# Optimization experiments

Measured on AMD Instinct MI355X. Metric: run time of the kernel, lower is better.

Reference implementation:

```python
import jax, jax.numpy as jnp
import numpy as np

CONV1_CH, CONV1_K = 8, 3
CONV2_CH, CONV2_K = 16, 2
DYN_POOL, MAX_POOL = 8, 4
FC1_IN, FC1_OUT = CONV2_CH * MAX_POOL * MAX_POOL, 100  # 256 -> 100


def k_max_pool(x, axis, k):
    # topk along axis, sort indices ascending, gather -> keeps original order of top-k
    xm = jnp.moveaxis(x, axis, -1)
    _, idx = jax.lax.top_k(xm, k)
    idx = jnp.sort(idx, axis=-1)
    out = jnp.take_along_axis(xm, idx, axis=-1)
    return jnp.moveaxis(out, -1, axis)


def _conv2d(x, w, b):
    y = jax.lax.conv_general_dilated(x, w, (1, 1), 'VALID',
                                     dimension_numbers=('NCHW', 'OIHW', 'NCHW'))
    return y + b[None, :, None, None]


def setup_inputs() -> dict:
    key = jax.random.key(0)
    ks = jax.random.split(key, 11)
    Lq, Ld, d, N = 128, 512, 64, 127
    inp = {
        'query': jax.random.normal(ks[0], (Lq, d), jnp.float32),
        'pos_doc': jax.random.normal(ks[1], (Ld, d), jnp.float32),
        'neg_docs': jax.random.normal(ks[2], (N, Ld, d), jnp.float32),
        'conv1_w': jax.random.normal(ks[3], (CONV1_CH, 1, CONV1_K, CONV1_K), jnp.float32) * 0.1,
        'conv1_b': jax.random.normal(ks[4], (CONV1_CH,), jnp.float32) * 0.1,
        'conv2_w': jax.random.normal(ks[5], (CONV2_CH, CONV1_CH, CONV2_K, CONV2_K), jnp.float32) * 0.1,
        'conv2_b': jax.random.normal(ks[6], (CONV2_CH,), jnp.float32) * 0.1,
        'lin1_w': jax.random.normal(ks[7], (FC1_OUT, FC1_IN), jnp.float32) * 0.05,
        'lin1_b': jax.random.normal(ks[8], (FC1_OUT,), jnp.float32) * 0.05,
        'lin2_w': jax.random.normal(ks[9], (1, FC1_OUT), jnp.float32) * 0.05,
        'lin2_b': jax.random.normal(ks[10], (1,), jnp.float32) * 0.05,
    }
    return inp


def reference(query, pos_doc, neg_docs, conv1_w, conv1_b, conv2_w, conv2_b,
              lin1_w, lin1_b, lin2_w, lin2_b):
    # Stack pos doc first, then negs (matches output stacking order in original)
    docs = jnp.concatenate([pos_doc[None], neg_docs], axis=0)      # [B, Ld, d]
    m = jnp.einsum('qd,bld->bql', query, docs)[:, None]            # [B, 1, Lq, Ld]
    # Layer 1: conv + relu + 2D k-max pooling to 8x8
    h = jax.nn.relu(_conv2d(m, conv1_w, conv1_b))                  # [B, 8, Lq-2, Ld-2]
    h = k_max_pool(h, 2, DYN_POOL)
    h = k_max_pool(h, 3, DYN_POOL)                                 # [B, 8, 8, 8]
    # Layer 2: conv + relu + 2D k-max pooling to 4x4
    h = jax.nn.relu(_conv2d(h, conv2_w, conv2_b))                  # [B, 16, 7, 7]
    h = k_max_pool(h, 2, MAX_POOL)
    h = k_max_pool(h, 3, MAX_POOL)                                 # [B, 16, 4, 4]
    feat = h.reshape(h.shape[0], -1)                               # [B, 256]
    z = jax.nn.relu(feat @ lin1_w.T + lin1_b)                      # [B, 100]
    s = jax.nn.relu(z @ lin2_w.T + lin2_b)                         # [B, 1]
    return s
```

## Files before the change

### kernel.cpp

```cpp
#include <hip/hip_runtime.h>
#include <cstdint>
#include <cstddef>

constexpr int kLq = 128;
constexpr int kLd = 512;
constexpr int kD  = 64;
constexpr int kB  = 128;
constexpr int kC1 = 8;
constexpr int kC2 = 16;
constexpr int kH1C = 510;
constexpr int kTileC = 51;
constexpr int kNTiles = 10;
constexpr int kMCols = 53;
constexpr int kNCand = kNTiles * 8;

constexpr int QT_PITCH = 132;
constexpr int DS_PITCH = 68;
constexpr int MS_PITCH = 57;

template <int K, bool LEX>
__device__ __forceinline__ void topk_insert(float (&tv)[K], int (&ti)[K],
                                            float v, int idx) {
  bool gK = LEX ? ((v > tv[K - 1]) | ((v == tv[K - 1]) & (idx < ti[K - 1])))
                : (v > tv[K - 1]);
  if (!gK) return;
  bool g[K];
#pragma unroll
  for (int k = 0; k < K; ++k)
    g[k] = LEX ? ((v > tv[k]) | ((v == tv[k]) & (idx < ti[k]))) : (v > tv[k]);
#pragma unroll
  for (int k = K - 1; k >= 1; --k) {
    tv[k] = g[k - 1] ? tv[k - 1] : (g[k] ? v : tv[k]);
    ti[k] = g[k - 1] ? ti[k - 1] : (g[k] ? idx : ti[k]);
  }
  if (g[0]) { tv[0] = v; ti[0] = idx; }
}

__global__ __launch_bounds__(512, 4)
void convpool1_kernel(const float* __restrict__ query,
                      const float* __restrict__ pos_doc,
                      const float* __restrict__ neg_docs,
                      const float* __restrict__ c1w,
                      const float* __restrict__ c1b,
                      float* __restrict__ candv,
                      int* __restrict__ candi) {
  __shared__ float q_t[64 * QT_PITCH];
  __shared__ float d_s[56 * DS_PITCH];
  __shared__ float m_s[kLq * MS_PITCH];
  float* ps = q_t;

  const int tid  = threadIdx.x;
  const int tile = blockIdx.x;
  const int b    = blockIdx.y;
  const int l0g  = tile * kTileC;

  const float* doc =
      (b == 0) ? pos_doc : (neg_docs + (size_t)(b - 1) * kLd * kD);

  {
    const float4* qf4 = reinterpret_cast<const float4*>(query);
    for (int e = tid; e < (kLq * kD) / 4; e += 512) {
      const int q  = e & 127;
      const int f4 = e >> 7;
      const float4 v = qf4[q * 16 + f4];
      const int d0 = f4 << 2;
      q_t[(d0 + 0) * QT_PITCH + q] = v.x;
      q_t[(d0 + 1) * QT_PITCH + q] = v.y;
      q_t[(d0 + 2) * QT_PITCH + q] = v.z;
      q_t[(d0 + 3) * QT_PITCH + q] = v.w;
    }
  }
  for (int e = tid; e < 56 * 16; e += 512) {
    const int l  = e >> 4;
    const int d0 = (e & 15) << 2;
    float4 v = make_float4(0.f, 0.f, 0.f, 0.f);
    if (l < kMCols)
      v = reinterpret_cast<const float4*>(doc + (size_t)(l0g + l) * kD)[e & 15];
    *reinterpret_cast<float4*>(&d_s[l * DS_PITCH + d0]) = v;
  }
  __syncthreads();

  if (tid < 32 * 14) {
    const int q0 = (tid & 31) << 2;
    const int l0 = (tid >> 5) << 2;
    float acc[4][4] = {};
#pragma unroll 4
    for (int d = 0; d < kD; d += 4) {
      float4 qv[4];
#pragma unroll
      for (int j = 0; j < 4; ++j)
        qv[j] = *reinterpret_cast<const float4*>(&q_t[(d + j) * QT_PITCH + q0]);
      float4 dv[4];
#pragma unroll
      for (int li = 0; li < 4; ++li)
        dv[li] = *reinterpret_cast<const float4*>(&d_s[(l0 + li) * DS_PITCH + d]);
#pragma unroll
      for (int li = 0; li < 4; ++li) {
        const float4 w = dv[li];
        acc[0][li] += qv[0].x * w.x + qv[1].x * w.y + qv[2].x * w.z + qv[3].x * w.w;
        acc[1][li] += qv[0].y * w.x + qv[1].y * w.y + qv[2].y * w.z + qv[3].y * w.w;
        acc[2][li] += qv[0].z * w.x + qv[1].z * w.y + qv[2].z * w.z + qv[3].z * w.w;
        acc[3][li] += qv[0].w * w.x + qv[1].w * w.y + qv[2].w * w.z + qv[3].w * w.w;
      }
    }
#pragma unroll
    for (int qi = 0; qi < 4; ++qi)
#pragma unroll
      for (int li = 0; li < 4; ++li)
        m_s[(q0 + qi) * MS_PITCH + (l0 + li)] = acc[qi][li];
  }
  __syncthreads();

  if (tid < kC1 * kTileC) {
    const int c = tid / kTileC;
    const int j = tid % kTileC;
    float w[9];
#pragma unroll
    for (int k = 0; k < 9; ++k) w[k] = c1w[c * 9 + k];
    const float bias = c1b[c];

    float tv[8]; int ti[8];
#pragma unroll
    for (int k = 0; k < 8; ++k) { tv[k] = -1.f; ti[k] = 0x7fffffff; }

    float acc01 = 0.f, s0_pend = 0.f;
    for (int t = 0; t < kLq; ++t) {
      const float x0 = m_s[t * MS_PITCH + j];
      const float x1 = m_s[t * MS_PITCH + j + 1];
      const float x2 = m_s[t * MS_PITCH + j + 2];
      const float S0 = w[0] * x0 + w[1] * x1 + w[2] * x2;
      const float S1 = w[3] * x0 + w[4] * x1 + w[5] * x2;
      const float S2 = w[6] * x0 + w[7] * x1 + w[8] * x2;
      if (t >= 2) {
        const float v = fmaxf(bias + acc01 + S2, 0.f);
        topk_insert<8, false>(tv, ti, v, t - 2);
      }
      acc01 = s0_pend + S1;
      s0_pend = S0;
    }
#pragma unroll
    for (int k = 0; k < 8; ++k) {
      int slot = 0;
#pragma unroll
      for (int m = 0; m < 8; ++m) slot += (ti[m] < ti[k]);
      ps[(c * 8 + slot) * 52 + j] = tv[k];
    }
  }
  __syncthreads();

  if (tid < 64) {
    const int g = tid;
    float tv[8]; int ti[8];
#pragma unroll
    for (int k = 0; k < 8; ++k) { tv[k] = -1.f; ti[k] = 0x7fffffff; }
    for (int j = 0; j < kTileC; ++j)
      topk_insert<8, false>(tv, ti, ps[g * 52 + j], l0g + j);
    float* cv = candv + ((size_t)b * 64 + g) * kNCand + tile * 8;
    int*   ci = candi + ((size_t)b * 64 + g) * kNCand + tile * 8;
#pragma unroll
    for (int k = 0; k < 8; ++k) {
      int slot = 0;
#pragma unroll
      for (int m = 0; m < 8; ++m) slot += (ti[m] < ti[k]);
      cv[slot] = tv[k];
      ci[slot] = ti[k];
    }
  }
}

__global__ __launch_bounds__(256, 4)
void tail_kernel(const float* __restrict__ candv, const int* __restrict__ candi,
                 const float* __restrict__ c2w, const float* __restrict__ c2b,
                 const float* __restrict__ l1w, const float* __restrict__ l1b,
                 const float* __restrict__ l2w, const float* __restrict__ l2b,
                 float* __restrict__ out) {
  __shared__ float mv[64][4][8];
  __shared__ int   mi[64][4][8];
  __shared__ float w2s[kC2 * kC1 * 4];
  __shared__ float b2s[kC2];
  __shared__ float h2in[kC1][8][8];
  __shared__ float h2o[kC2][7][7];
  __shared__ float h3[kC2][4][7];
  __shared__ __align__(16) float feat[256];
  __shared__ float zbuf[100];

  const int b = blockIdx.x, tid = threadIdx.x;

  for (int e = tid; e < kC2 * kC1 * 4; e += 256) w2s[e] = c2w[e];
  if (tid < kC2) b2s[tid] = c2b[tid];

  {
    const int g = tid >> 2, lane4 = tid & 3;
    const float* cv = candv + ((size_t)b * 64 + g) * kNCand;
    const int*   ci = candi + ((size_t)b * 64 + g) * kNCand;
    float tv[8]; int ti[8];
#pragma unroll
    for (int k = 0; k < 8; ++k) { tv[k] = -1.f; ti[k] = 0x7fffffff; }
    for (int p = lane4; p < kNCand; p += 4)
      topk_insert<8, false>(tv, ti, cv[p], ci[p]);
#pragma unroll
    for (int k = 0; k < 8; ++k) { mv[g][lane4][k] = tv[k]; mi[g][lane4][k] = ti[k]; }
  }
  __syncthreads();
  if ((tid & 3) == 0) {
    const int g = tid >> 2;
    const int c = g >> 3, row = g & 7;
    float tv[8]; int ti[8];
#pragma unroll
    for (int k = 0; k < 8; ++k) { tv[k] = -1.f; ti[k] = 0x7fffffff; }
#pragma unroll
    for (int li = 0; li < 4; ++li)
#pragma unroll
      for (int kk = 0; kk < 8; ++kk)
        topk_insert<8, true>(tv, ti, mv[g][li][kk], mi[g][li][kk]);
#pragma unroll
    for (int k = 0; k < 8; ++k) {
      int slot = 0;
#pragma unroll
      for (int m = 0; m < 8; ++m) slot += (ti[m] < ti[k]);
      h2in[c][row][slot] = tv[k];
    }
  }
  __syncthreads();

  for (int v = tid; v < kC2 * 49; v += 256) {
    const int c2 = v / 49;
    const int r  = (v % 49) / 7;
    const int j  = v % 7;
    float s = b2s[c2];
#pragma unroll
    for (int cin = 0; cin < kC1; ++cin) {
      const float* wp = &w2s[(c2 * kC1 + cin) * 4];
      s += wp[0] * h2in[cin][r][j]     + wp[1] * h2in[cin][r][j + 1];
      s += wp[2] * h2in[cin][r + 1][j] + wp[3] * h2in[cin][r + 1][j + 1];
    }
    h2o[c2][r][j] = fmaxf(s, 0.f);
  }
  __syncthreads();

  for (int p = tid; p < kC2 * 7; p += 256) {
    const int c2 = p / 7, j = p % 7;
    float tv[4]; int ti[4];
#pragma unroll
    for (int k = 0; k < 4; ++k) { tv[k] = -1.f; ti[k] = 0x7fffffff; }
    for (int r = 0; r < 7; ++r) topk_insert<4, false>(tv, ti, h2o[c2][r][j], r);
#pragma unroll
    for (int k = 0; k < 4; ++k) {
      int slot = 0;
#pragma unroll
      for (int m = 0; m < 4; ++m) slot += (ti[m] < ti[k]);
      h3[c2][slot][j] = tv[k];
    }
  }
  __syncthreads();

  for (int p = tid; p < kC2 * 4; p += 256) {
    const int c2 = p >> 2, r = p & 3;
    float tv[4]; int ti[4];
#pragma unroll
    for (int k = 0; k < 4; ++k) { tv[k] = -1.f; ti[k] = 0x7fffffff; }
    for (int j = 0; j < 7; ++j) topk_insert<4, false>(tv, ti, h3[c2][r][j], j);
#pragma unroll
    for (int k = 0; k < 4; ++k) {
      int slot = 0;
#pragma unroll
      for (int m = 0; m < 4; ++m) slot += (ti[m] < ti[k]);
      feat[c2 * 16 + r * 4 + slot] = tv[k];
    }
  }
  __syncthreads();

  for (int o = tid; o < 100; o += 256) {
    float s = l1b[o];
    const float4* wr = reinterpret_cast<const float4*>(l1w + (size_t)o * 256);
    const float4* fr = reinterpret_cast<const float4*>(feat);
    for (int i = 0; i < 64; ++i) {
      const float4 w = wr[i], f = fr[i];
      s += w.x * f.x + w.y * f.y + w.z * f.z + w.w * f.w;
    }
    zbuf[o] = fmaxf(s, 0.f);
  }
  __syncthreads();

  if (tid < 64) {
    float s = 0.f;
    for (int o = tid; o < 100; o += 64) s += zbuf[o] * l2w[o];
#pragma unroll
    for (int off = 32; off >= 1; off >>= 1) s += __shfl_down(s, off, 64);
    if (tid == 0) out[b] = fmaxf(s + l2b[0], 0.f);
  }
}

extern "C" void kernel_launch(void* const* d_in, const int* in_sizes, int n_in,
                              void* d_out, int out_size, void* d_ws,
                              size_t ws_size, hipStream_t stream) {
  const float* query    = (const float*)d_in[0];
  const float* pos_doc  = (const float*)d_in[1];
  const float* neg_docs = (const float*)d_in[2];
  const float* c1w      = (const float*)d_in[3];
  const float* c1b      = (const float*)d_in[4];
  const float* c2w      = (const float*)d_in[5];
  const float* c2b      = (const float*)d_in[6];
  const float* l1w      = (const float*)d_in[7];
  const float* l1b      = (const float*)d_in[8];
  const float* l2w      = (const float*)d_in[9];
  const float* l2b      = (const float*)d_in[10];
  float* out = (float*)d_out;

  float* candv = (float*)d_ws;
  int*   candi = (int*)((char*)d_ws + (size_t)kB * 64 * kNCand * sizeof(float));

  dim3 gridA(kNTiles, kB);
  hipLaunchKernelGGL(convpool1_kernel, gridA, dim3(512), 0, stream,
                     query, pos_doc, neg_docs, c1w, c1b, candv, candi);
  hipLaunchKernelGGL(tail_kernel, dim3(kB), dim3(256), 0, stream,
                     candv, candi, c2w, c2b, l1w, l1b, l2w, l2b, out);
}
```

Before: 310.9 us.

## Alias LDS buffers in convpool1 and widen tail top-k merge to 8 lanes

The first kernel puts its score matrix in the same LDS region as the transposed query, which cuts shared memory per block so more blocks can be resident. An extra barrier keeps the accumulators in registers until every thread has finished reading q_t, and the launch bound asks for 6 blocks per SM. The tail kernel moves to 512 threads, with 8 lanes per row building partial top-8 lists that are merged in a tree instead of by one serial thread. This adds barriers and register pressure, and the 6-wave occupancy target may force spills.

```diff
diff --git a/kernel.cpp b/kernel.cpp
--- a/kernel.cpp
+++ b/kernel.cpp
@@ -18,6 +18,12 @@
 constexpr int DS_PITCH = 68;
 constexpr int MS_PITCH = 57;
 
+constexpr int kQtOff = 0;
+constexpr int kDsOff = 64 * QT_PITCH;
+constexpr int kMsOff = 0;
+constexpr int kPsOff = kLq * MS_PITCH;
+constexpr int kLdsFloats = kDsOff + 56 * DS_PITCH;
+
 template <int K, bool LEX>
 __device__ __forceinline__ void topk_insert(float (&tv)[K], int (&ti)[K],
                                             float v, int idx) {
@@ -36,7 +42,7 @@
   if (g[0]) { tv[0] = v; ti[0] = idx; }
 }
 
-__global__ __launch_bounds__(512, 4)
+__global__ __launch_bounds__(512, 6)
 void convpool1_kernel(const float* __restrict__ query,
                       const float* __restrict__ pos_doc,
                       const float* __restrict__ neg_docs,
@@ -44,10 +50,11 @@
                       const float* __restrict__ c1b,
                       float* __restrict__ candv,
                       int* __restrict__ candi) {
-  __shared__ float q_t[64 * QT_PITCH];
-  __shared__ float d_s[56 * DS_PITCH];
-  __shared__ float m_s[kLq * MS_PITCH];
-  float* ps = q_t;
+  __shared__ float lds[kLdsFloats];
+  float* q_t = lds + kQtOff;
+  float* d_s = lds + kDsOff;
+  float* m_s = lds + kMsOff;
+  float* ps  = lds + kPsOff;
 
   const int tid  = threadIdx.x;
   const int tile = blockIdx.x;
@@ -80,10 +87,10 @@
   }
   __syncthreads();
 
+  float acc[4][4] = {};
   if (tid < 32 * 14) {
     const int q0 = (tid & 31) << 2;
     const int l0 = (tid >> 5) << 2;
-    float acc[4][4] = {};
 #pragma unroll 4
     for (int d = 0; d < kD; d += 4) {
       float4 qv[4];
@@ -103,6 +110,11 @@
         acc[3][li] += qv[0].w * w.x + qv[1].w * w.y + qv[2].w * w.z + qv[3].w * w.w;
       }
     }
+  }
+  __syncthreads();
+  if (tid < 32 * 14) {
+    const int q0 = (tid & 31) << 2;
+    const int l0 = (tid >> 5) << 2;
 #pragma unroll
     for (int qi = 0; qi < 4; ++qi)
 #pragma unroll
@@ -168,14 +180,14 @@
   }
 }
 
-__global__ __launch_bounds__(256, 4)
+__global__ __launch_bounds__(512)
 void tail_kernel(const float* __restrict__ candv, const int* __restrict__ candi,
                  const float* __restrict__ c2w, const float* __restrict__ c2b,
                  const float* __restrict__ l1w, const float* __restrict__ l1b,
                  const float* __restrict__ l2w, const float* __restrict__ l2b,
                  float* __restrict__ out) {
-  __shared__ float mv[64][4][8];
-  __shared__ int   mi[64][4][8];
+  __shared__ float mv[64][8][8];
+  __shared__ int   mi[64][8][8];
   __shared__ float w2s[kC2 * kC1 * 4];
   __shared__ float b2s[kC2];
   __shared__ float h2in[kC1][8][8];
@@ -186,33 +198,38 @@
 
   const int b = blockIdx.x, tid = threadIdx.x;
 
-  for (int e = tid; e < kC2 * kC1 * 4; e += 256) w2s[e] = c2w[e];
+  if (tid < kC2 * kC1 * 4) w2s[tid] = c2w[tid];
   if (tid < kC2) b2s[tid] = c2b[tid];
 
+  const int g = tid >> 3, lane8 = tid & 7;
+  float tv[8]; int ti[8];
+#pragma unroll
+  for (int k = 0; k < 8; ++k) { tv[k] = -1.f; ti[k] = 0x7fffffff; }
   {
-    const int g = tid >> 2, lane4 = tid & 3;
     const float* cv = candv + ((size_t)b * 64 + g) * kNCand;
     const int*   ci = candi + ((size_t)b * 64 + g) * kNCand;
-    float tv[8]; int ti[8];
-#pragma unroll
-    for (int k = 0; k < 8; ++k) { tv[k] = -1.f; ti[k] = 0x7fffffff; }
-    for (int p = lane4; p < kNCand; p += 4)
+    for (int p = lane8; p < kNCand; p += 8)
       topk_insert<8, false>(tv, ti, cv[p], ci[p]);
 #pragma unroll
-    for (int k = 0; k < 8; ++k) { mv[g][lane4][k] = tv[k]; mi[g][lane4][k] = ti[k]; }
-  }
-  __syncthreads();
-  if ((tid & 3) == 0) {
-    const int g = tid >> 2;
+    for (int k = 0; k < 8; ++k) { mv[g][lane8][k] = tv[k]; mi[g][lane8][k] = ti[k]; }
+  }
+  __syncthreads();
+
+#pragma unroll
+  for (int s = 4; s >= 1; s >>= 1) {
+    if (lane8 < s) {
+#pragma unroll
+      for (int kk = 0; kk < 8; ++kk)
+        topk_insert<8, true>(tv, ti, mv[g][lane8 + s][kk], mi[g][lane8 + s][kk]);
+      if (s > 1) {
+#pragma unroll
+        for (int k = 0; k < 8; ++k) { mv[g][lane8][k] = tv[k]; mi[g][lane8][k] = ti[k]; }
+      }
+    }
+    __syncthreads();
+  }
+  if (lane8 == 0) {
     const int c = g >> 3, row = g & 7;
-    float tv[8]; int ti[8];
-#pragma unroll
-    for (int k = 0; k < 8; ++k) { tv[k] = -1.f; ti[k] = 0x7fffffff; }
-#pragma unroll
-    for (int li = 0; li < 4; ++li)
-#pragma unroll
-      for (int kk = 0; kk < 8; ++kk)
-        topk_insert<8, true>(tv, ti, mv[g][li][kk], mi[g][li][kk]);
 #pragma unroll
     for (int k = 0; k < 8; ++k) {
       int slot = 0;
@@ -223,7 +240,7 @@
   }
   __syncthreads();
 
-  for (int v = tid; v < kC2 * 49; v += 256) {
+  for (int v = tid; v < kC2 * 49; v += 512) {
     const int c2 = v / 49;
     const int r  = (v % 49) / 7;
     const int j  = v % 7;
@@ -238,39 +255,40 @@
   }
   __syncthreads();
 
-  for (int p = tid; p < kC2 * 7; p += 256) {
-    const int c2 = p / 7, j = p % 7;
-    float tv[4]; int ti[4];
-#pragma unroll
-    for (int k = 0; k < 4; ++k) { tv[k] = -1.f; ti[k] = 0x7fffffff; }
-    for (int r = 0; r < 7; ++r) topk_insert<4, false>(tv, ti, h2o[c2][r][j], r);
+  if (tid < kC2 * 7) {
+    const int c2 = tid / 7, j = tid % 7;
+    float tv4[4]; int ti4[4];
+#pragma unroll
+    for (int k = 0; k < 4; ++k) { tv4[k] = -1.f; ti4[k] = 0x7fffffff; }
+    for (int r = 0; r < 7; ++r) topk_insert<4, false>(tv4, ti4, h2o[c2][r][j], r);
 #pragma unroll
     for (int k = 0; k < 4; ++k) {
       int slot = 0;
 #pragma unroll
-      for (int m = 0; m < 4; ++m) slot += (ti[m] < ti[k]);
-      h3[c2][slot][j] = tv[k];
-    }
-  }
-  __syncthreads();
-
-  for (int p = tid; p < kC2 * 4; p += 256) {
-    const int c2 = p >> 2, r = p & 3;
-    float tv[4]; int ti[4];
-#pragma unroll
-    for (int k = 0; k < 4; ++k) { tv[k] = -1.f; ti[k] = 0x7fffffff; }
-    for (int j = 0; j < 7; ++j) topk_insert<4, false>(tv, ti, h3[c2][r][j], j);
+      for (int m = 0; m < 4; ++m) slot += (ti4[m] < ti4[k]);
+      h3[c2][slot][j] = tv4[k];
+    }
+  }
+  __syncthreads();
+
+  if (tid < kC2 * 4) {
+    const int c2 = tid >> 2, r = tid & 3;
+    float tv4[4]; int ti4[4];
+#pragma unroll
+    for (int k = 0; k < 4; ++k) { tv4[k] = -1.f; ti4[k] = 0x7fffffff; }
+    for (int j = 0; j < 7; ++j) topk_insert<4, false>(tv4, ti4, h3[c2][r][j], j);
 #pragma unroll
     for (int k = 0; k < 4; ++k) {
       int slot = 0;
 #pragma unroll
-      for (int m = 0; m < 4; ++m) slot += (ti[m] < ti[k]);
-      feat[c2 * 16 + r * 4 + slot] = tv[k];
-    }
-  }
-  __syncthreads();
-
-  for (int o = tid; o < 100; o += 256) {
+      for (int m = 0; m < 4; ++m) slot += (ti4[m] < ti4[k]);
+      feat[c2 * 16 + r * 4 + slot] = tv4[k];
+    }
+  }
+  __syncthreads();
+
+  if (tid < 100) {
+    const int o = tid;
     float s = l1b[o];
     const float4* wr = reinterpret_cast<const float4*>(l1w + (size_t)o * 256);
     const float4* fr = reinterpret_cast<const float4*>(feat);
@@ -313,6 +331,6 @@
   dim3 gridA(kNTiles, kB);
   hipLaunchKernelGGL(convpool1_kernel, gridA, dim3(512), 0, stream,
                      query, pos_doc, neg_docs, c1w, c1b, candv, candi);
-  hipLaunchKernelGGL(tail_kernel, dim3(kB), dim3(256), 0, stream,
+  hipLaunchKernelGGL(tail_kernel, dim3(kB), dim3(512), 0, stream,
                      candv, candi, c2w, c2b, l1w, l1b, l2w, l2b, out);
 }
```

New measurement: 270.8 us. -12.9%, faster.
